# Kernel tuning notes

Hardware: AMD Instinct MI355X
Metric: run time of the kernel (lower is better)

Reference implementation:

```python
import math
import jax, jax.numpy as jnp
import numpy as np

B, S, H, DQ, DV = 2, 2048, 16, 192, 128
NEG_INF = jnp.float32(-1e30)


def setup_inputs() -> dict:
    key = jax.random.key(0)
    kq, kk, kv = jax.random.split(key, 3)
    q = jax.random.normal(kq, (B, S, H, DQ), dtype=jnp.float32)
    k = jax.random.normal(kk, (B, S, H, DQ), dtype=jnp.float32)
    v = jax.random.normal(kv, (B, S, H, DV), dtype=jnp.float32)
    return {"q": q, "k": k, "v": v}


def reference(q, k, v):
    # Causal MLA attention, BSHD layout, asymmetric QK vs V head dims.
    dq = q.shape[-1]
    scale = jnp.asarray(math.sqrt(1.0 / dq), dtype=q.dtype)  # default 1/sqrt(dq)
    # scores: [B, H, S, S]
    scores = jnp.einsum("bqhd,bkhd->bhqk", q, k) * scale
    s = q.shape[1]
    causal = jnp.tril(jnp.ones((s, s), dtype=bool))  # qidx >= kidx
    scores = jnp.where(causal[None, None, :, :], scores, NEG_INF)
    p = jax.nn.softmax(scores, axis=-1)
    # out: [B, S, H, DV]
    out = jnp.einsum("bhqk,bkhd->bqhd", p, v)
    return out
```

## Files before the change

kernel.cpp:

```cpp
#include <hip/hip_runtime.h>

#define B_ 2
#define S_ 2048
#define H_ 16
#define DQ_ 192
#define DV_ 128
#define SCL2 0.10411163731422901f

typedef short short8 __attribute__((ext_vector_type(8)));
typedef float f32x4 __attribute__((ext_vector_type(4)));
typedef float f32x16 __attribute__((ext_vector_type(16)));
typedef unsigned uint2v __attribute__((ext_vector_type(2)));

#define KG_BYTES ((size_t)25165824)
#define VG_BYTES ((size_t)16777216)

__device__ __forceinline__ unsigned short f2bf(float f) {
  union { float f; unsigned u; } x; x.f = f;
  unsigned r = x.u + 0x7FFFu + ((x.u >> 16) & 1u);
  return (unsigned short)(r >> 16);
}

__device__ __forceinline__ float hw_exp2(float x) {
  float r; asm("v_exp_f32 %0, %1" : "=v"(r) : "v"(x)); return r;
}
__device__ __forceinline__ unsigned cvtpk(float lo, float hi) {
  unsigned r; asm("v_cvt_pk_bf16_f32 %0, %1, %2" : "=v"(r) : "v"(lo), "v"(hi)); return r;
}
__device__ __forceinline__ float pl32max(float x) {
  uint2v r = __builtin_amdgcn_permlane32_swap(__float_as_uint(x), __float_as_uint(x), false, false);
  return fmaxf(__uint_as_float(r[0]), __uint_as_float(r[1]));
}
__device__ __forceinline__ float pl32add(float x) {
  uint2v r = __builtin_amdgcn_permlane32_swap(__float_as_uint(x), __float_as_uint(x), false, false);
  return __uint_as_float(r[0]) + __uint_as_float(r[1]);
}

#define GLL16(src, dst) \
  __builtin_amdgcn_global_load_lds((const __attribute__((address_space(1))) void*)(src), \
                                   (__attribute__((address_space(3))) void*)(dst), 16, 0, 0)

__global__ __launch_bounds__(256) void prep_k(const float* __restrict__ K,
                                              unsigned short* __restrict__ Kg) {
  int idx = blockIdx.x * 256 + threadIdx.x;
  int d4 = idx % 48; int r = idx / 48;
  int h = r % H_; r /= H_;
  int s = r % S_; int b = r / S_;
  float4 f = *(const float4*)(K + (size_t)((b * S_ + s) * H_ + h) * DQ_ + d4 * 4);
  ushort4 u; u.x = f2bf(f.x); u.y = f2bf(f.y); u.z = f2bf(f.z); u.w = f2bf(f.w);
  size_t rowb = (size_t)((b * H_ + h) * S_ + s) * (DQ_ * 2);
  int cb = (d4 * 8) ^ ((s & 7) << 4);
  *(ushort4*)((char*)Kg + rowb + cb) = u;
}

__global__ __launch_bounds__(256) void prep_v(const float* __restrict__ V,
                                              unsigned short* __restrict__ Vg) {
  __shared__ float lv[64][132];
  int blk = blockIdx.x;
  int tile = blk & 31, bh = blk >> 5;
  int b = bh >> 4, h = bh & 15;
  int tid = threadIdx.x;
  #pragma unroll
  for (int it = 0; it < 8; ++it) {
    int idx = it * 256 + tid;
    int s_in = idx >> 5, d4 = idx & 31;
    float4 f = *(const float4*)(V + (size_t)((b * S_ + tile * 64 + s_in) * H_ + h) * DV_ + d4 * 4);
    lv[s_in][d4 * 4 + 0] = f.x; lv[s_in][d4 * 4 + 1] = f.y;
    lv[s_in][d4 * 4 + 2] = f.z; lv[s_in][d4 * 4 + 3] = f.w;
  }
  __syncthreads();
  char* base = (char*)Vg + (size_t)blk * 16384;
  #pragma unroll
  for (int it = 0; it < 4; ++it) {
    int ch = it * 256 + tid;
    int pr = ch >> 4, ci = ch & 15;
    int orig = ci ^ (pr & 15);
    int dv = pr * 2 + (orig >> 3);
    int k0 = (orig & 7) * 8;
    short8 u;
    #pragma unroll
    for (int e = 0; e < 8; ++e) u[e] = (short)f2bf(lv[k0 + e][dv]);
    *(short8*)(base + ch * 16) = u;
  }
}

__launch_bounds__(512, 1)
__global__ void mla_fwd(const float* __restrict__ Q,
                        const unsigned short* __restrict__ Kg,
                        const unsigned short* __restrict__ Vg,
                        float* __restrict__ O) {
  __shared__ __align__(16) unsigned char SB[3][40960];

  const int tid  = threadIdx.x;
  const int wid  = tid >> 6;
  const int lane = tid & 63;
  const int l31  = lane & 31;
  const int hi   = lane >> 5;
  const int hi16 = hi * 16;
  const int qg   = wid & 3;
  const int kh   = wid >> 2;

  const int i  = blockIdx.x;
  const int x  = i & 7;
  const int li = i >> 3;
  const int bh = x * 4 + (li >> 3);
  const int jj = li & 7;
  const int b  = bh >> 4, h = bh & 15;

  const char* kg_bh = (const char*)Kg + (size_t)bh * S_ * (DQ_ * 2);
  const char* vg_bh = (const char*)Vg + (size_t)bh * 32 * 16384;

  const int kxor = (lane & 7) << 4;
  const int prl  = l31 >> 1;
  const int nb_  = (lane & 1) * 8 + hi;
  int voff[2];
  #pragma unroll
  for (int ks = 0; ks < 2; ++ks) {
    int n = nb_ + kh * 4 + ks * 2;
    voff[ks] = prl * 256 + ((n ^ prl) << 4);
  }

  #define STAGE(buf, t)                                                           \
    do {                                                                          \
      const char* kba = kg_bh + (size_t)(t) * 24576 + wid * 5120 + lane * 16;     \
      const char* vba = vg_bh + (size_t)(t) * 16384 - 24576 + wid * 5120 + lane * 16; \
      _Pragma("unroll")                                                           \
      for (int ci = 0; ci < 5; ++ci) {                                            \
        const int cc = wid * 5 + ci;                                              \
        const char* src = (cc < 24) ? (kba + ci * 1024) : (vba + ci * 1024);      \
        GLL16(src, &SB[buf][cc * 1024]);                                          \
      }                                                                           \
    } while (0)

  for (int job = 0; job < 2; ++job) {
    const int qt  = job ? jj : (15 - jj);
    const int wq0 = qt * 128 + qg * 32;
    const int qln = wq0 + l31;

    short8 qf[12];
    {
      const size_t qoff = (size_t)((b * S_ + qln) * H_ + h) * DQ_;
      #pragma unroll
      for (int d0 = 0; d0 < 12; ++d0) {
        const float* p = Q + qoff + d0 * 16 + hi * 8;
        float4 f0 = *(const float4*)(p);
        float4 f1 = *(const float4*)(p + 4);
        short8 a;
        a[0] = f2bf(f0.x * SCL2); a[1] = f2bf(f0.y * SCL2);
        a[2] = f2bf(f0.z * SCL2); a[3] = f2bf(f0.w * SCL2);
        a[4] = f2bf(f1.x * SCL2); a[5] = f2bf(f1.y * SCL2);
        a[6] = f2bf(f1.z * SCL2); a[7] = f2bf(f1.w * SCL2);
        qf[d0] = a;
      }
    }

    f32x16 o4[4];
    #pragma unroll
    for (int t2 = 0; t2 < 4; ++t2) o4[t2] = (f32x16)0.0f;
    float m = -1e30f, l = 0.0f;

    const int ntiles = 2 * qt + 2;

    STAGE(0, 0);
    if (ntiles > 1) STAGE(1, 1);

    int bc = 0;
    for (int kt = 0; kt < ntiles; ++kt) {
      if (kt + 1 < ntiles) asm volatile("s_waitcnt vmcnt(10)" ::: "memory");
      else                 asm volatile("s_waitcnt vmcnt(0)" ::: "memory");
      __builtin_amdgcn_s_barrier();
      if (kt + 2 < ntiles) {
        int bs = bc - 1; if (bs < 0) bs = 2;
        STAGE(bs, kt + 2);
      }

      const int kbase = kt * 64;
      const int khb = kbase + kh * 32;

      if (khb <= wq0 + 31) {
        const char* kr = (const char*)&SB[bc][0] + (kh * 32 + l31) * 384;
        f32x16 s = (f32x16)0.0f;
        __builtin_amdgcn_s_setprio(1);
        #pragma unroll
        for (int d0 = 0; d0 < 12; ++d0) {
          const int col = (d0 * 32 + hi16) ^ kxor;
          s = __builtin_amdgcn_mfma_f32_32x32x16_bf16(*(const short8*)(kr + col), qf[d0], s, 0, 0, 0);
        }
        __builtin_amdgcn_s_setprio(0);

        const char* vb = (const char*)&SB[bc][0] + 24576;
        short8 v00 = *(const short8*)(vb + 0 * 4096 + voff[0]);
        short8 v01 = *(const short8*)(vb + 0 * 4096 + voff[1]);
        short8 v10 = *(const short8*)(vb + 1 * 4096 + voff[0]);
        short8 v11 = *(const short8*)(vb + 1 * 4096 + voff[1]);
        short8 v20 = *(const short8*)(vb + 2 * 4096 + voff[0]);
        short8 v21 = *(const short8*)(vb + 2 * 4096 + voff[1]);
        short8 v30 = *(const short8*)(vb + 3 * 4096 + voff[0]);
        short8 v31 = *(const short8*)(vb + 3 * 4096 + voff[1]);

        float p_[16];
        #pragma unroll
        for (int r = 0; r < 16; ++r) p_[r] = s[r];
        if (khb + 31 > wq0) {
          const int rem = qln - khb - 4 * hi;
          #pragma unroll
          for (int r = 0; r < 16; ++r) {
            const int kof = (r & 3) + 8 * (r >> 2);
            if (kof > rem) p_[r] = -1e30f;
          }
        }

        float t8[8];
        #pragma unroll
        for (int r = 0; r < 8; ++r) t8[r] = fmaxf(p_[r], p_[8 + r]);
        float t4[4];
        #pragma unroll
        for (int r = 0; r < 4; ++r) t4[r] = fmaxf(t8[r], t8[4 + r]);
        float mx = fmaxf(fmaxf(t4[0], t4[1]), fmaxf(t4[2], t4[3]));
        mx = pl32max(mx);
        if (__any(mx > m + 8.0f)) {
          float mn = fmaxf(m, mx);
          float al = hw_exp2(m - mn);
          #pragma unroll
          for (int t2 = 0; t2 < 4; ++t2) o4[t2] *= al;
          l *= al; m = mn;
        }
        #pragma unroll
        for (int rr = 0; rr < 16; ++rr) p_[rr] = hw_exp2(p_[rr] - m);
        float a8[8];
        #pragma unroll
        for (int r = 0; r < 8; ++r) a8[r] = p_[r] + p_[8 + r];
        float a4[4];
        #pragma unroll
        for (int r = 0; r < 4; ++r) a4[r] = a8[r] + a8[4 + r];
        l += (a4[0] + a4[1]) + (a4[2] + a4[3]);

        unsigned a_ = cvtpk(p_[0], p_[1]),   b2_ = cvtpk(p_[2], p_[3]);
        unsigned c_ = cvtpk(p_[4], p_[5]),   d_  = cvtpk(p_[6], p_[7]);
        unsigned e_ = cvtpk(p_[8], p_[9]),   f_  = cvtpk(p_[10], p_[11]);
        unsigned g_ = cvtpk(p_[12], p_[13]), h_  = cvtpk(p_[14], p_[15]);
        uint2v s02 = __builtin_amdgcn_permlane32_swap(a_, c_, false, false);
        uint2v s13 = __builtin_amdgcn_permlane32_swap(b2_, d_, false, false);
        uint2v s46 = __builtin_amdgcn_permlane32_swap(e_, g_, false, false);
        uint2v s57 = __builtin_amdgcn_permlane32_swap(f_, h_, false, false);
        union { unsigned u[4]; short8 s; } pb0, pb1;
        pb0.u[0] = s02[0]; pb0.u[1] = s13[0]; pb0.u[2] = s02[1]; pb0.u[3] = s13[1];
        pb1.u[0] = s46[0]; pb1.u[1] = s57[0]; pb1.u[2] = s46[1]; pb1.u[3] = s57[1];

        __builtin_amdgcn_s_setprio(1);
        o4[0] = __builtin_amdgcn_mfma_f32_32x32x16_bf16(v00, pb0.s, o4[0], 0, 0, 0);
        o4[0] = __builtin_amdgcn_mfma_f32_32x32x16_bf16(v01, pb1.s, o4[0], 0, 0, 0);
        o4[1] = __builtin_amdgcn_mfma_f32_32x32x16_bf16(v10, pb0.s, o4[1], 0, 0, 0);
        o4[1] = __builtin_amdgcn_mfma_f32_32x32x16_bf16(v11, pb1.s, o4[1], 0, 0, 0);
        o4[2] = __builtin_amdgcn_mfma_f32_32x32x16_bf16(v20, pb0.s, o4[2], 0, 0, 0);
        o4[2] = __builtin_amdgcn_mfma_f32_32x32x16_bf16(v21, pb1.s, o4[2], 0, 0, 0);
        o4[3] = __builtin_amdgcn_mfma_f32_32x32x16_bf16(v30, pb0.s, o4[3], 0, 0, 0);
        o4[3] = __builtin_amdgcn_mfma_f32_32x32x16_bf16(v31, pb1.s, o4[3], 0, 0, 0);
        __builtin_amdgcn_s_setprio(0);
      }

      ++bc; if (bc == 3) bc = 0;
    }

    float lr = pl32add(l);
    __syncthreads();
    char* mrg = (char*)&SB[0][0];
    if (kh == 1) {
      float* po = (float*)(mrg + qg * 17408 + lane * 272);
      #pragma unroll
      for (int t2 = 0; t2 < 4; ++t2) {
        #pragma unroll
        for (int rr = 0; rr < 4; ++rr) {
          float4 st = { o4[t2][rr * 4 + 0], o4[t2][rr * 4 + 1],
                        o4[t2][rr * 4 + 2], o4[t2][rr * 4 + 3] };
          *(float4*)(po + t2 * 16 + rr * 4) = st;
        }
      }
      float* pm = (float*)(mrg + 69632 + (qg * 64 + lane) * 8);
      pm[0] = m; pm[1] = lr;
    }
    __syncthreads();
    if (kh == 0) {
      const float* po = (const float*)(mrg + qg * 17408 + lane * 272);
      const float* pm = (const float*)(mrg + 69632 + (qg * 64 + lane) * 8);
      const float mB = pm[0], lB = pm[1];
      const float ms = fmaxf(m, mB);
      const float wA = hw_exp2(m - ms), wB = hw_exp2(mB - ms);
      const float inv = 1.0f / (lr * wA + lB * wB);
      float* ob = O + (size_t)((b * S_ + qln) * H_ + h) * DV_;
      #pragma unroll
      for (int t2 = 0; t2 < 4; ++t2) {
        #pragma unroll
        for (int rr = 0; rr < 4; ++rr) {
          float4 vb4 = *(const float4*)(po + t2 * 16 + rr * 4);
          float4 st = { (o4[t2][rr * 4 + 0] * wA + vb4.x * wB) * inv,
                        (o4[t2][rr * 4 + 1] * wA + vb4.y * wB) * inv,
                        (o4[t2][rr * 4 + 2] * wA + vb4.z * wB) * inv,
                        (o4[t2][rr * 4 + 3] * wA + vb4.w * wB) * inv };
          *(float4*)(ob + t2 * 32 + rr * 8 + hi * 4) = st;
        }
      }
    }
    __syncthreads();
  }
  #undef STAGE
}

__launch_bounds__(256)
__global__ void mla_fwd_fb(const float* __restrict__ Q,
                           const float* __restrict__ K,
                           const float* __restrict__ V,
                           float* __restrict__ O) {
  __shared__ __align__(16) unsigned short Kl[2][32][200];
  __shared__ __align__(16) unsigned short Vt[2][128][40];
  __shared__ __align__(16) unsigned short Pl[4][16][40];
  const int tid = threadIdx.x, wid = tid >> 6, lane = tid & 63;
  const int l15 = lane & 15, g = lane >> 4;
  const int qtile = (int)gridDim.x - 1 - (int)blockIdx.x;
  const int bh = blockIdx.y, b = bh >> 4, h = bh & 15;
  const int q0w = qtile * 64 + wid * 16;
  const int krs = H_ * DQ_, vrs = H_ * DV_;
  short8 aq[6];
  {
    const int qoff = ((b * S_ + (q0w + l15)) * H_ + h) * DQ_;
    #pragma unroll
    for (int d0 = 0; d0 < 6; ++d0) {
      const float* p = Q + qoff + d0 * 32 + g * 8;
      float4 f0 = *(const float4*)(p); float4 f1 = *(const float4*)(p + 4);
      short8 a;
      a[0]=f2bf(f0.x); a[1]=f2bf(f0.y); a[2]=f2bf(f0.z); a[3]=f2bf(f0.w);
      a[4]=f2bf(f1.x); a[5]=f2bf(f1.y); a[6]=f2bf(f1.z); a[7]=f2bf(f1.w);
      aq[d0] = a;
    }
  }
  f32x4 o[8];
  #pragma unroll
  for (int t = 0; t < 8; ++t) o[t] = (f32x4)0.0f;
  float m[4], l[4];
  #pragma unroll
  for (int r = 0; r < 4; ++r) { m[r] = -1e30f; l[r] = 0.0f; }
  const int ntiles = qtile * 2 + 2;
  float4 kr[6], vr[4];
  {
    const float* Kb = K + ((b * S_) * H_ + h) * DQ_;
    #pragma unroll
    for (int i = 0; i < 6; ++i) { int idx = i*256+tid; int row = idx/48, c4 = idx%48;
      kr[i] = *(const float4*)(Kb + row*krs + c4*4); }
    const float* Vb = V + ((b * S_) * H_ + h) * DV_;
    #pragma unroll
    for (int i = 0; i < 4; ++i) { int idx = i*256+tid; int row = idx&31, c4 = idx>>5;
      vr[i] = *(const float4*)(Vb + row*vrs + c4*4); }
    #pragma unroll
    for (int i = 0; i < 6; ++i) { int idx = i*256+tid; int row = idx/48, c4 = idx%48;
      ushort4 u; u.x=f2bf(kr[i].x); u.y=f2bf(kr[i].y); u.z=f2bf(kr[i].z); u.w=f2bf(kr[i].w);
      *(ushort4*)&Kl[0][row][c4*4] = u; }
    #pragma unroll
    for (int i = 0; i < 4; ++i) { int idx = i*256+tid; int row = idx&31, c4 = idx>>5;
      Vt[0][c4*4+0][row]=f2bf(vr[i].x); Vt[0][c4*4+1][row]=f2bf(vr[i].y);
      Vt[0][c4*4+2][row]=f2bf(vr[i].z); Vt[0][c4*4+3][row]=f2bf(vr[i].w); }
  }
  __syncthreads();
  int cur = 0;
  for (int kt = 0; kt < ntiles; ++kt) {
    const int kbase = kt * 32;
    const bool pf = (kt + 1 < ntiles);
    if (pf) {
      const int nb = kbase + 32;
      const float* Kb = K + ((b*S_+nb)*H_ + h)*DQ_;
      #pragma unroll
      for (int i = 0; i < 6; ++i) { int idx = i*256+tid; int row = idx/48, c4 = idx%48;
        kr[i] = *(const float4*)(Kb + row*krs + c4*4); }
      const float* Vb = V + ((b*S_+nb)*H_ + h)*DV_;
      #pragma unroll
      for (int i = 0; i < 4; ++i) { int idx = i*256+tid; int row = idx&31, c4 = idx>>5;
        vr[i] = *(const float4*)(Vb + row*vrs + c4*4); }
    }
    f32x4 sa0 = (f32x4)0.0f, sa1 = (f32x4)0.0f;
    #pragma unroll
    for (int d0 = 0; d0 < 6; ++d0) {
      short8 b0 = *(const short8*)&Kl[cur][l15][d0*32 + g*8];
      sa0 = __builtin_amdgcn_mfma_f32_16x16x32_bf16(aq[d0], b0, sa0, 0, 0, 0);
      short8 b1 = *(const short8*)&Kl[cur][16+l15][d0*32 + g*8];
      sa1 = __builtin_amdgcn_mfma_f32_16x16x32_bf16(aq[d0], b1, sa1, 0, 0, 0);
    }
    float p0[4], p1[4];
    #pragma unroll
    for (int r = 0; r < 4; ++r) {
      const int qg = q0w + 4*g + r;
      float s0 = sa0[r]*SCL2, s1 = sa1[r]*SCL2;
      if (kbase + l15 > qg) s0 = -1e30f;
      if (kbase + 16 + l15 > qg) s1 = -1e30f;
      p0[r] = s0; p1[r] = s1;
    }
    #pragma unroll
    for (int r = 0; r < 4; ++r) {
      float rm = fmaxf(p0[r], p1[r]);
      #pragma unroll
      for (int off = 1; off < 16; off <<= 1) rm = fmaxf(rm, __shfl_xor(rm, off));
      float mn = fmaxf(m[r], rm);
      float alpha = exp2f(m[r] - mn); m[r] = mn;
      float e0 = exp2f(p0[r] - mn), e1 = exp2f(p1[r] - mn);
      p0[r] = e0; p1[r] = e1;
      float rsum = e0 + e1;
      #pragma unroll
      for (int off = 1; off < 16; off <<= 1) rsum += __shfl_xor(rsum, off);
      l[r] = l[r]*alpha + rsum;
      #pragma unroll
      for (int t = 0; t < 8; ++t) o[t][r] *= alpha;
    }
    #pragma unroll
    for (int r = 0; r < 4; ++r) {
      Pl[wid][4*g+r][l15]      = f2bf(p0[r]);
      Pl[wid][4*g+r][16+l15]   = f2bf(p1[r]);
    }
    short8 pa = *(const short8*)&Pl[wid][l15][g*8];
    #pragma unroll
    for (int t = 0; t < 8; ++t) {
      short8 vb = *(const short8*)&Vt[cur][t*16+l15][g*8];
      o[t] = __builtin_amdgcn_mfma_f32_16x16x32_bf16(pa, vb, o[t], 0, 0, 0);
    }
    if (pf) {
      #pragma unroll
      for (int i = 0; i < 6; ++i) { int idx = i*256+tid; int row = idx/48, c4 = idx%48;
        ushort4 u; u.x=f2bf(kr[i].x); u.y=f2bf(kr[i].y); u.z=f2bf(kr[i].z); u.w=f2bf(kr[i].w);
        *(ushort4*)&Kl[cur^1][row][c4*4] = u; }
      #pragma unroll
      for (int i = 0; i < 4; ++i) { int idx = i*256+tid; int row = idx&31, c4 = idx>>5;
        Vt[cur^1][c4*4+0][row]=f2bf(vr[i].x); Vt[cur^1][c4*4+1][row]=f2bf(vr[i].y);
        Vt[cur^1][c4*4+2][row]=f2bf(vr[i].z); Vt[cur^1][c4*4+3][row]=f2bf(vr[i].w); }
    }
    __syncthreads();
    cur ^= 1;
  }
  #pragma unroll
  for (int r = 0; r < 4; ++r) {
    const int qg = q0w + 4*g + r;
    const float inv = 1.0f / l[r];
    #pragma unroll
    for (int t = 0; t < 8; ++t)
      O[((b*S_+qg)*H_ + h)*DV_ + t*16 + l15] = o[t][r] * inv;
  }
}

extern "C" void kernel_launch(void* const* d_in, const int* in_sizes, int n_in,
                              void* d_out, int out_size, void* d_ws, size_t ws_size,
                              hipStream_t stream) {
  const float* q = (const float*)d_in[0];
  const float* k = (const float*)d_in[1];
  const float* v = (const float*)d_in[2];
  float* out = (float*)d_out;

  if (ws_size >= KG_BYTES + VG_BYTES) {
    unsigned short* Kg = (unsigned short*)d_ws;
    unsigned short* Vg = (unsigned short*)((char*)d_ws + KG_BYTES);
    prep_k<<<dim3((B_ * S_ * H_ * 48) / 256), dim3(256), 0, stream>>>(k, Kg);
    prep_v<<<dim3(B_ * H_ * 32), dim3(256), 0, stream>>>(v, Vg);
    mla_fwd<<<dim3(256), dim3(512), 0, stream>>>(q, Kg, Vg, out);
  } else {
    dim3 grid(S_ / 64, B_ * H_);
    mla_fwd_fb<<<grid, dim3(256), 0, stream>>>(q, k, v, out);
  }
}
```

Measured before the change: 90.77 us.

## Software-pipeline QK^T of next tile ahead of softmax and PV of current tile

Restructures the attention loop so the QK^T MFMAs for tile r+1 are issued before the softmax and PV of tile r, letting matrix work overlap with the exponent and reduction VALU work. QK^T is split into two independent accumulator chains to shorten the MFMA dependency chain, and half of the V LDS reads are deferred. The loop now waits for all outstanding global loads each iteration because the next tile must be resident, which reduces effective prefetch depth and raises register pressure.

```diff
diff --git a/kernel.cpp b/kernel.cpp
--- a/kernel.cpp
+++ b/kernel.cpp
@@ -132,6 +132,22 @@
       }                                                                           \
     } while (0)
 
+  #define QKT(dst, bb)                                                            \
+    {                                                                             \
+      const char* kr_ = (const char*)&SB[bb][0] + (kh * 32 + l31) * 384;          \
+      f32x16 sa_ = (f32x16)0.0f, sb_ = (f32x16)0.0f;                              \
+      __builtin_amdgcn_s_setprio(1);                                              \
+      _Pragma("unroll")                                                           \
+      for (int d0 = 0; d0 < 12; d0 += 2) {                                        \
+        const int c0 = (d0 * 32 + hi16) ^ kxor;                                   \
+        const int c1 = (d0 * 32 + 32 + hi16) ^ kxor;                              \
+        sa_ = __builtin_amdgcn_mfma_f32_32x32x16_bf16(*(const short8*)(kr_ + c0), qf[d0],     sa_, 0, 0, 0); \
+        sb_ = __builtin_amdgcn_mfma_f32_32x32x16_bf16(*(const short8*)(kr_ + c1), qf[d0 + 1], sb_, 0, 0, 0); \
+      }                                                                           \
+      __builtin_amdgcn_s_setprio(0);                                              \
+      dst = sa_ + sb_;                                                            \
+    }
+
   for (int job = 0; job < 2; ++job) {
     const int qt  = job ? jj : (15 - jj);
     const int wq0 = qt * 128 + qg * 32;
@@ -159,63 +175,56 @@
     for (int t2 = 0; t2 < 4; ++t2) o4[t2] = (f32x16)0.0f;
     float m = -1e30f, l = 0.0f;
 
-    const int ntiles = 2 * qt + 2;
+    const int nt = 2 * qt + 2;
 
     STAGE(0, 0);
-    if (ntiles > 1) STAGE(1, 1);
-
-    int bc = 0;
-    for (int kt = 0; kt < ntiles; ++kt) {
-      if (kt + 1 < ntiles) asm volatile("s_waitcnt vmcnt(10)" ::: "memory");
-      else                 asm volatile("s_waitcnt vmcnt(0)" ::: "memory");
+    STAGE(1, 1);
+    asm volatile("s_waitcnt vmcnt(5)" ::: "memory");
+    __builtin_amdgcn_s_barrier();
+    f32x16 sp;
+    const bool act0 = (kh * 32 <= wq0 + 31);
+    if (act0) QKT(sp, 0);
+
+    for (int r = 0; r < nt; ++r) {
+      const int bc = r % 3;
+      const int bn = (r + 1) % 3;
+
+      asm volatile("s_waitcnt vmcnt(0)" ::: "memory");
       __builtin_amdgcn_s_barrier();
-      if (kt + 2 < ntiles) {
-        int bs = bc - 1; if (bs < 0) bs = 2;
-        STAGE(bs, kt + 2);
-      }
-
-      const int kbase = kt * 64;
-      const int khb = kbase + kh * 32;
-
-      if (khb <= wq0 + 31) {
-        const char* kr = (const char*)&SB[bc][0] + (kh * 32 + l31) * 384;
-        f32x16 s = (f32x16)0.0f;
-        __builtin_amdgcn_s_setprio(1);
-        #pragma unroll
-        for (int d0 = 0; d0 < 12; ++d0) {
-          const int col = (d0 * 32 + hi16) ^ kxor;
-          s = __builtin_amdgcn_mfma_f32_32x32x16_bf16(*(const short8*)(kr + col), qf[d0], s, 0, 0, 0);
-        }
-        __builtin_amdgcn_s_setprio(0);
-
+      if (r + 2 < nt) STAGE((r + 2) % 3, r + 2);
+
+      const int khb = r * 64 + kh * 32;
+      const bool actR = (khb <= wq0 + 31);
+      const bool nxA  = (r + 1 < nt) && (khb + 64 <= wq0 + 31);
+
+      f32x16 sn;
+      if (nxA) QKT(sn, bn);
+
+      if (actR) {
         const char* vb = (const char*)&SB[bc][0] + 24576;
         short8 v00 = *(const short8*)(vb + 0 * 4096 + voff[0]);
         short8 v01 = *(const short8*)(vb + 0 * 4096 + voff[1]);
         short8 v10 = *(const short8*)(vb + 1 * 4096 + voff[0]);
         short8 v11 = *(const short8*)(vb + 1 * 4096 + voff[1]);
-        short8 v20 = *(const short8*)(vb + 2 * 4096 + voff[0]);
-        short8 v21 = *(const short8*)(vb + 2 * 4096 + voff[1]);
-        short8 v30 = *(const short8*)(vb + 3 * 4096 + voff[0]);
-        short8 v31 = *(const short8*)(vb + 3 * 4096 + voff[1]);
 
         float p_[16];
         #pragma unroll
-        for (int r = 0; r < 16; ++r) p_[r] = s[r];
+        for (int rr = 0; rr < 16; ++rr) p_[rr] = sp[rr];
         if (khb + 31 > wq0) {
           const int rem = qln - khb - 4 * hi;
           #pragma unroll
-          for (int r = 0; r < 16; ++r) {
-            const int kof = (r & 3) + 8 * (r >> 2);
-            if (kof > rem) p_[r] = -1e30f;
+          for (int rr = 0; rr < 16; ++rr) {
+            const int kof = (rr & 3) + 8 * (rr >> 2);
+            if (kof > rem) p_[rr] = -1e30f;
           }
         }
 
         float t8[8];
         #pragma unroll
-        for (int r = 0; r < 8; ++r) t8[r] = fmaxf(p_[r], p_[8 + r]);
+        for (int rr = 0; rr < 8; ++rr) t8[rr] = fmaxf(p_[rr], p_[8 + rr]);
         float t4[4];
         #pragma unroll
-        for (int r = 0; r < 4; ++r) t4[r] = fmaxf(t8[r], t8[4 + r]);
+        for (int rr = 0; rr < 4; ++rr) t4[rr] = fmaxf(t8[rr], t8[4 + rr]);
         float mx = fmaxf(fmaxf(t4[0], t4[1]), fmaxf(t4[2], t4[3]));
         mx = pl32max(mx);
         if (__any(mx > m + 8.0f)) {
@@ -229,10 +238,10 @@
         for (int rr = 0; rr < 16; ++rr) p_[rr] = hw_exp2(p_[rr] - m);
         float a8[8];
         #pragma unroll
-        for (int r = 0; r < 8; ++r) a8[r] = p_[r] + p_[8 + r];
+        for (int rr = 0; rr < 8; ++rr) a8[rr] = p_[rr] + p_[8 + rr];
         float a4[4];
         #pragma unroll
-        for (int r = 0; r < 4; ++r) a4[r] = a8[r] + a8[4 + r];
+        for (int rr = 0; rr < 4; ++rr) a4[rr] = a8[rr] + a8[4 + rr];
         l += (a4[0] + a4[1]) + (a4[2] + a4[3]);
 
         unsigned a_ = cvtpk(p_[0], p_[1]),   b2_ = cvtpk(p_[2], p_[3]);
@@ -247,6 +256,11 @@
         pb0.u[0] = s02[0]; pb0.u[1] = s13[0]; pb0.u[2] = s02[1]; pb0.u[3] = s13[1];
         pb1.u[0] = s46[0]; pb1.u[1] = s57[0]; pb1.u[2] = s46[1]; pb1.u[3] = s57[1];
 
+        short8 v20 = *(const short8*)(vb + 2 * 4096 + voff[0]);
+        short8 v21 = *(const short8*)(vb + 2 * 4096 + voff[1]);
+        short8 v30 = *(const short8*)(vb + 3 * 4096 + voff[0]);
+        short8 v31 = *(const short8*)(vb + 3 * 4096 + voff[1]);
+
         __builtin_amdgcn_s_setprio(1);
         o4[0] = __builtin_amdgcn_mfma_f32_32x32x16_bf16(v00, pb0.s, o4[0], 0, 0, 0);
         o4[0] = __builtin_amdgcn_mfma_f32_32x32x16_bf16(v01, pb1.s, o4[0], 0, 0, 0);
@@ -259,7 +273,7 @@
         __builtin_amdgcn_s_setprio(0);
       }
 
-      ++bc; if (bc == 3) bc = 0;
+      if (nxA) sp = sn;
     }
 
     float lr = pl32add(l);
@@ -304,6 +318,7 @@
     __syncthreads();
   }
   #undef STAGE
+  #undef QKT
 }
 
 __launch_bounds__(256)
```

New measurement: 96.40 us. +6.2%, slower.
